# Kernel tuning notes

Hardware: AMD Instinct MI355X
Metric: run time of the kernel (lower is better)

Reference implementation:

```python
import jax, jax.numpy as jnp
import numpy as np

CUTOFF = 10.0
CUTOFF_SR = 4.0
KEHALF = 7.199822675975274
OFFSET2 = 1.0
N_ATOMS = 100000
N_EDGES = 3200000


def switch_fn(d):
    # smooth poly5 switch: 1 at d=0, 0 at d>=cutoff_short_range
    x = d / CUTOFF_SR
    s = 1.0 - x * x * x * (10.0 - 15.0 * x + 6.0 * x * x)
    return jnp.where(x < 1.0, s, 0.0)


def setup_inputs() -> dict:
    key = jax.random.key(0)
    k1, k2, k3, k4, k5, k6 = jax.random.split(key, 6)
    atomic_charges = jax.random.normal(k1, (N_ATOMS,), dtype=jnp.float32)
    atomic_dipoles = jax.random.normal(k2, (N_ATOMS, 3), dtype=jnp.float32)
    atomic_quadrupoles = jax.random.normal(k3, (N_ATOMS, 3, 3), dtype=jnp.float32)
    vectors_uv = 3.0 * jax.random.normal(k4, (N_EDGES, 3), dtype=jnp.float32)
    distances_uv = jnp.linalg.norm(vectors_uv, axis=-1)  # consistent, >0, some > cutoff
    idx_u = jax.random.randint(k5, (N_EDGES,), 0, N_ATOMS, dtype=jnp.int32)
    idx_v = jax.random.randint(k6, (N_EDGES,), 0, N_ATOMS, dtype=jnp.int32)
    return {
        'atomic_charges': atomic_charges,
        'atomic_dipoles': atomic_dipoles,
        'atomic_quadrupoles': atomic_quadrupoles,
        'vectors_uv': vectors_uv,
        'distances_uv': distances_uv,
        'idx_u': idx_u,
        'idx_v': idx_v,
    }


def reference(atomic_charges, atomic_dipoles, atomic_quadrupoles,
              vectors_uv, distances_uv, idx_u, idx_v):
    d = distances_uv                                  # [E]
    d_damped = jnp.sqrt(d * d + OFFSET2)
    sw = switch_fn(d)
    chi = sw / d_damped + (1.0 - sw) / d
    cutoff2 = CUTOFF * CUTOFF
    chi_shift = 2.0 / CUTOFF - d / cutoff2

    q_u = atomic_charges[idx_u]                       # [E]
    q_v = atomic_charges[idx_v]
    Eelec = q_u * q_v * (chi - chi_shift)

    chi2 = chi * chi
    chi3 = chi2 * chi
    cutoff3 = cutoff2 * CUTOFF
    cutoff4 = cutoff3 * CUTOFF
    chi2_shift = 3.0 / cutoff2 - 2.0 * d / cutoff3
    chi3_shift = 4.0 / cutoff3 - 3.0 * d / cutoff4

    # dipole contributions
    nvec = vectors_uv / d[:, None]                    # [E,3] normalized
    dip_u = atomic_dipoles[idx_u]
    dip_v = atomic_dipoles[idx_v]
    dot_uv = jnp.sum(nvec * dip_v, axis=1)
    dot_vu = jnp.sum(nvec * dip_u, axis=1)
    Eelec_cd = 2.0 * q_u * dot_uv * (chi2 - chi2_shift)
    Eelec_dd = (jnp.sum(dip_u * dip_v, axis=1) - 3.0 * dot_uv * dot_vu) * (chi3 - chi3_shift)
    Eelec = Eelec + Eelec_cd + Eelec_dd

    # quadrupole contributions
    outer = vectors_uv[:, :, None] * vectors_uv[:, None, :]      # [E,3,3]
    trace_mean = jnp.trace(outer, axis1=-2, axis2=-1) / 3.0      # [E]
    traceless = outer - trace_mean[:, None, None] * jnp.eye(3, dtype=outer.dtype)
    traceless = traceless / (d * d)[:, None, None]
    quad_v = atomic_quadrupoles[idx_v]                           # [E,3,3]
    sum_uv = jnp.sum(traceless * quad_v, axis=(1, 2))
    Eelec = Eelec + q_u * sum_uv * (chi3 - chi3_shift)

    Eelec = KEHALF * Eelec
    return jnp.where(d <= CUTOFF, Eelec, jnp.zeros_like(Eelec))
```

## Files before the change

kernel.cpp:

```cpp
#include <hip/hip_runtime.h>
#include <hip/hip_fp16.h>


#define CUTOFF      10.0f
#define KEHALF      7.199822675975274f

typedef float    f32x4 __attribute__((ext_vector_type(4)));
typedef unsigned u32x4 __attribute__((ext_vector_type(4)));

__device__ __forceinline__ unsigned pack_h2(float a, float b) {
    return __builtin_bit_cast(unsigned, __floats2half2_rn(a, b));
}
__device__ __forceinline__ float2 unpack_h2(unsigned u) {
    return __half22float2(__builtin_bit_cast(__half2, u));
}

__global__ __launch_bounds__(256) void pack_atoms_kernel(
    const float* __restrict__ q,
    const float* __restrict__ dip,
    const float* __restrict__ quad,
    f32x4* __restrict__ table,
    int N)
{
    int i = blockIdx.x * blockDim.x + threadIdx.x;
    if (i >= N) return;
    const float* dp = dip + 3 * (size_t)i;
    const float* qp = quad + 9 * (size_t)i;

    f32x4 w0 = {q[i], dp[0], dp[1], dp[2]};

    float q00 = qp[0], q01 = qp[1], q02 = qp[2];
    float q10 = qp[3], q11 = qp[4], q12 = qp[5];
    float q20 = qp[6], q21 = qp[7], q22 = qp[8];
    float trQ3 = (q00 + q11 + q22) * (1.0f / 3.0f);

    u32x4 w1 = {pack_h2(q00 - trQ3, q11 - trQ3),
                pack_h2(q22 - trQ3, q01 + q10),
                pack_h2(q02 + q20, q12 + q21),
                0u};

    table[2 * (size_t)i + 0] = w0;
    table[2 * (size_t)i + 1] = __builtin_bit_cast(f32x4, w1);
}

__device__ __forceinline__ float edge_energy(
    float vx, float vy, float vz,
    f32x4 au, f32x4 av, u32x4 bv)
{
    float d2 = vx * vx + vy * vy + vz * vz;
    float d = sqrtf(d2);
    float inv_d = 1.0f / d;
    float inv_d2 = inv_d * inv_d;

    float x = d * 0.25f;
    float x2 = x * x;
    float x3 = x2 * x;
    float sw = 1.0f - x3 * (10.0f - 15.0f * x + 6.0f * x2);
    sw = (x < 1.0f) ? sw : 0.0f;
    float chi = sw * rsqrtf(d2 + 1.0f) + (1.0f - sw) * inv_d;

    float c1 = chi - (0.2f   - 0.01f   * d);
    float chi2 = chi * chi;
    float chi3 = chi2 * chi;
    float c2 = chi2 - (0.03f  - 0.002f  * d);
    float c3 = chi3 - (0.004f - 0.0003f * d);

    float qu = au.x, qv = av.x;
    float Ee = qu * qv * c1;

    float dot_uv = (vx * av.y + vy * av.z + vz * av.w) * inv_d;
    float dot_vu = (vx * au.y + vy * au.z + vz * au.w) * inv_d;
    float dd     = au.y * av.y + au.z * av.z + au.w * av.w;

    Ee += 2.0f * qu * dot_uv * c2;
    Ee += (dd - 3.0f * dot_uv * dot_vu) * c3;

    float2 h0 = unpack_h2(bv.x);
    float2 h1 = unpack_h2(bv.y);
    float2 h2 = unpack_h2(bv.z);
    float num = h0.x * vx * vx + h0.y * vy * vy + h1.x * vz * vz
              + h1.y * vx * vy + h2.x * vx * vz + h2.y * vy * vz;
    Ee += qu * (num * inv_d2) * c3;

    Ee *= KEHALF;
    return (d <= CUTOFF) ? Ee : 0.0f;
}

__global__ __launch_bounds__(256) void damped_elec_pipe(
    const f32x4* __restrict__ table,
    const float* __restrict__ vec,
    const int*   __restrict__ idx_u,
    const int*   __restrict__ idx_v,
    float*       __restrict__ out,
    int E)
{
    int tid = blockIdx.x * blockDim.x + threadIdx.x;
    int stride = gridDim.x * blockDim.x;

    size_t i = tid;
    if (i >= (size_t)E) return;

    int u = __builtin_nontemporal_load(idx_u + i);
    int v = __builtin_nontemporal_load(idx_v + i);
    float vx = __builtin_nontemporal_load(vec + 3 * i + 0);
    float vy = __builtin_nontemporal_load(vec + 3 * i + 1);
    float vz = __builtin_nontemporal_load(vec + 3 * i + 2);

    for (;;) {
        size_t inext = i + (size_t)stride;
        bool more = inext < (size_t)E;

        f32x4 au = table[2 * (size_t)u];
        f32x4 av = table[2 * (size_t)v + 0];
        f32x4 bq = table[2 * (size_t)v + 1];

        int un = 0, vn = 0;
        float nx = 0.f, ny = 0.f, nz = 0.f;
        if (more) {
            un = __builtin_nontemporal_load(idx_u + inext);
            vn = __builtin_nontemporal_load(idx_v + inext);
            nx = __builtin_nontemporal_load(vec + 3 * inext + 0);
            ny = __builtin_nontemporal_load(vec + 3 * inext + 1);
            nz = __builtin_nontemporal_load(vec + 3 * inext + 2);
        }

        float r = edge_energy(vx, vy, vz, au, av, __builtin_bit_cast(u32x4, bq));
        __builtin_nontemporal_store(r, out + i);

        if (!more) break;
        i = inext;
        u = un; v = vn; vx = nx; vy = ny; vz = nz;
    }
}

__global__ __launch_bounds__(256) void damped_elec_unpacked(
    const float* __restrict__ q,
    const float* __restrict__ dip,
    const float* __restrict__ quad,
    const float* __restrict__ vec,
    const int*   __restrict__ idx_u,
    const int*   __restrict__ idx_v,
    float*       __restrict__ out,
    int E)
{
    int i = blockIdx.x * blockDim.x + threadIdx.x;
    if (i >= E) return;
    float vx = vec[3 * (size_t)i + 0];
    float vy = vec[3 * (size_t)i + 1];
    float vz = vec[3 * (size_t)i + 2];
    int u = idx_u[i];
    int v = idx_v[i];
    const float* pu = dip + 3 * (size_t)u;
    const float* pv = dip + 3 * (size_t)v;
    const float* pq = quad + 9 * (size_t)v;

    f32x4 au = {q[u], pu[0], pu[1], pu[2]};
    f32x4 av = {q[v], pv[0], pv[1], pv[2]};
    float trQ3 = (pq[0] + pq[4] + pq[8]) * (1.0f / 3.0f);
    u32x4 bv = {pack_h2(pq[0] - trQ3, pq[4] - trQ3),
                pack_h2(pq[8] - trQ3, pq[1] + pq[3]),
                pack_h2(pq[2] + pq[6], pq[5] + pq[7]),
                0u};
    out[i] = edge_energy(vx, vy, vz, au, av, bv);
}

extern "C" void kernel_launch(void* const* d_in, const int* in_sizes, int n_in,
                              void* d_out, int out_size, void* d_ws, size_t ws_size,
                              hipStream_t stream) {
    const float* q    = (const float*)d_in[0];
    const float* dip  = (const float*)d_in[1];
    const float* quad = (const float*)d_in[2];
    const float* vec  = (const float*)d_in[3];
    const int*   iu   = (const int*)d_in[5];
    const int*   iv   = (const int*)d_in[6];
    float* out = (float*)d_out;

    int N = in_sizes[0];
    int E = in_sizes[4];
    int block = 256;

    size_t need = (size_t)N * 32;
    if (ws_size >= need) {
        f32x4* table = (f32x4*)d_ws;
        int pgrid = (N + block - 1) / block;
        pack_atoms_kernel<<<pgrid, block, 0, stream>>>(q, dip, quad, table, N);
        int egrid = 2048;
        damped_elec_pipe<<<egrid, block, 0, stream>>>(table, vec, iu, iv, out, E);
    } else {
        int egrid = (E + block - 1) / block;
        damped_elec_unpacked<<<egrid, block, 0, stream>>>(q, dip, quad, vec, iu, iv, out, E);
    }
}
```

Before: 56.38 us.

## Deepen software pipeline to two stages and use raw rsq intrinsics

The grid-stride edge loop becomes a two-stage software pipeline. Edge indices and vectors are prefetched two iterations ahead, and the gathered atom-table rows one iteration ahead, so gather latency overlaps with the energy arithmetic. The distance math also switches from sqrt plus reciprocal to the hardware rsq intrinsic, with d derived as d2*rsq. This adds register pressure and loses some precision in d and 1/d.

After: 56.74 us. About the same (+0.6%).

```diff
diff --git a/kernel.cpp b/kernel.cpp
--- a/kernel.cpp
+++ b/kernel.cpp
@@ -2,7 +2,6 @@
 #include <hip/hip_fp16.h>
 
 
-#define CUTOFF      10.0f
 #define KEHALF      7.199822675975274f
 
 typedef float    f32x4 __attribute__((ext_vector_type(4)));
@@ -45,11 +44,13 @@
 
 __device__ __forceinline__ float edge_energy(
     float vx, float vy, float vz,
-    f32x4 au, f32x4 av, u32x4 bv)
-{
+    f32x4 au, f32x4 av, f32x4 bqf)
+{
+    u32x4 bv = __builtin_bit_cast(u32x4, bqf);
+
     float d2 = vx * vx + vy * vy + vz * vz;
-    float d = sqrtf(d2);
-    float inv_d = 1.0f / d;
+    float inv_d = __builtin_amdgcn_rsqf(d2);
+    float d = d2 * inv_d;
     float inv_d2 = inv_d * inv_d;
 
     float x = d * 0.25f;
@@ -57,7 +58,7 @@
     float x3 = x2 * x;
     float sw = 1.0f - x3 * (10.0f - 15.0f * x + 6.0f * x2);
     sw = (x < 1.0f) ? sw : 0.0f;
-    float chi = sw * rsqrtf(d2 + 1.0f) + (1.0f - sw) * inv_d;
+    float chi = sw * __builtin_amdgcn_rsqf(d2 + 1.0f) + (1.0f - sw) * inv_d;
 
     float c1 = chi - (0.2f   - 0.01f   * d);
     float chi2 = chi * chi;
@@ -83,10 +84,10 @@
     Ee += qu * (num * inv_d2) * c3;
 
     Ee *= KEHALF;
-    return (d <= CUTOFF) ? Ee : 0.0f;
-}
-
-__global__ __launch_bounds__(256) void damped_elec_pipe(
+    return (d <= 10.0f) ? Ee : 0.0f;
+}
+
+__global__ __launch_bounds__(256) void damped_elec_pipe2(
     const f32x4* __restrict__ table,
     const float* __restrict__ vec,
     const int*   __restrict__ idx_u,
@@ -94,42 +95,62 @@
     float*       __restrict__ out,
     int E)
 {
-    int tid = blockIdx.x * blockDim.x + threadIdx.x;
-    int stride = gridDim.x * blockDim.x;
-
-    size_t i = tid;
-    if (i >= (size_t)E) return;
-
-    int u = __builtin_nontemporal_load(idx_u + i);
-    int v = __builtin_nontemporal_load(idx_v + i);
-    float vx = __builtin_nontemporal_load(vec + 3 * i + 0);
-    float vy = __builtin_nontemporal_load(vec + 3 * i + 1);
-    float vz = __builtin_nontemporal_load(vec + 3 * i + 2);
+    const int tid = blockIdx.x * blockDim.x + threadIdx.x;
+    const int stride = gridDim.x * blockDim.x;
+
+    int i0 = tid;
+    if (i0 >= E) return;
+
+    int u0 = __builtin_nontemporal_load(idx_u + i0);
+    int v0 = __builtin_nontemporal_load(idx_v + i0);
+    float ax = __builtin_nontemporal_load(vec + 3 * (size_t)i0 + 0);
+    float ay = __builtin_nontemporal_load(vec + 3 * (size_t)i0 + 1);
+    float az = __builtin_nontemporal_load(vec + 3 * (size_t)i0 + 2);
+    f32x4 au0 = table[2 * (size_t)u0];
+    f32x4 av0 = table[2 * (size_t)v0 + 0];
+    f32x4 bq0 = table[2 * (size_t)v0 + 1];
+
+    int i1 = i0 + stride;
+    bool has1 = i1 < E;
+    int u1 = 0, v1 = 0;
+    float bx = 0.f, by = 0.f, bz = 0.f;
+    if (has1) {
+        u1 = __builtin_nontemporal_load(idx_u + i1);
+        v1 = __builtin_nontemporal_load(idx_v + i1);
+        bx = __builtin_nontemporal_load(vec + 3 * (size_t)i1 + 0);
+        by = __builtin_nontemporal_load(vec + 3 * (size_t)i1 + 1);
+        bz = __builtin_nontemporal_load(vec + 3 * (size_t)i1 + 2);
+    }
 
     for (;;) {
-        size_t inext = i + (size_t)stride;
-        bool more = inext < (size_t)E;
-
-        f32x4 au = table[2 * (size_t)u];
-        f32x4 av = table[2 * (size_t)v + 0];
-        f32x4 bq = table[2 * (size_t)v + 1];
-
-        int un = 0, vn = 0;
-        float nx = 0.f, ny = 0.f, nz = 0.f;
-        if (more) {
-            un = __builtin_nontemporal_load(idx_u + inext);
-            vn = __builtin_nontemporal_load(idx_v + inext);
-            nx = __builtin_nontemporal_load(vec + 3 * inext + 0);
-            ny = __builtin_nontemporal_load(vec + 3 * inext + 1);
-            nz = __builtin_nontemporal_load(vec + 3 * inext + 2);
+        f32x4 au1 = {}, av1 = {}, bq1 = {};
+        if (has1) {
+            au1 = table[2 * (size_t)u1];
+            av1 = table[2 * (size_t)v1 + 0];
+            bq1 = table[2 * (size_t)v1 + 1];
         }
 
-        float r = edge_energy(vx, vy, vz, au, av, __builtin_bit_cast(u32x4, bq));
-        __builtin_nontemporal_store(r, out + i);
-
-        if (!more) break;
-        i = inext;
-        u = un; v = vn; vx = nx; vy = ny; vz = nz;
+        int i2 = i1 + stride;
+        bool has2 = has1 && (i2 < E);
+        int u2 = 0, v2 = 0;
+        float cx = 0.f, cy = 0.f, cz = 0.f;
+        if (has2) {
+            u2 = __builtin_nontemporal_load(idx_u + i2);
+            v2 = __builtin_nontemporal_load(idx_v + i2);
+            cx = __builtin_nontemporal_load(vec + 3 * (size_t)i2 + 0);
+            cy = __builtin_nontemporal_load(vec + 3 * (size_t)i2 + 1);
+            cz = __builtin_nontemporal_load(vec + 3 * (size_t)i2 + 2);
+        }
+
+        float r = edge_energy(ax, ay, az, au0, av0, bq0);
+        __builtin_nontemporal_store(r, out + i0);
+
+        if (!has1) break;
+
+        i0 = i1; ax = bx; ay = by; az = bz;
+        au0 = au1; av0 = av1; bq0 = bq1;
+        i1 = i2; u1 = u2; v1 = v2; bx = cx; by = cy; bz = cz;
+        has1 = has2;
     }
 }
 
@@ -161,7 +182,7 @@
                 pack_h2(pq[8] - trQ3, pq[1] + pq[3]),
                 pack_h2(pq[2] + pq[6], pq[5] + pq[7]),
                 0u};
-    out[i] = edge_energy(vx, vy, vz, au, av, bv);
+    out[i] = edge_energy(vx, vy, vz, au, av, __builtin_bit_cast(f32x4, bv));
 }
 
 extern "C" void kernel_launch(void* const* d_in, const int* in_sizes, int n_in,
@@ -184,8 +205,7 @@
         f32x4* table = (f32x4*)d_ws;
         int pgrid = (N + block - 1) / block;
         pack_atoms_kernel<<<pgrid, block, 0, stream>>>(q, dip, quad, table, N);
-        int egrid = 2048;
-        damped_elec_pipe<<<egrid, block, 0, stream>>>(table, vec, iu, iv, out, E);
+        damped_elec_pipe2<<<2048, block, 0, stream>>>(table, vec, iu, iv, out, E);
     } else {
         int egrid = (E + block - 1) / block;
         damped_elec_unpacked<<<egrid, block, 0, stream>>>(q, dip, quad, vec, iu, iv, out, E);
```
